# Kernel tuning notes

Hardware: AMD Instinct MI355X
Metric: run time of the kernel (lower is better)

Reference implementation:

```python
import jax, jax.numpy as jnp
import numpy as np

NUM_HEADS = 4
NUM_GROUPS = 8
EPS = 1e-5


def setup_inputs() -> dict:
    key = jax.random.key(0)
    ks = jax.random.split(key, 7)
    B, C, T, H, W = 2, 256, 16, 16, 16
    return {
        "x": jax.random.normal(ks[0], (B, C, T, H, W), dtype=jnp.float32),
        "norm_w": jax.random.normal(ks[1], (C,), dtype=jnp.float32),
        "norm_b": jax.random.normal(ks[2], (C,), dtype=jnp.float32),
        "qkv_w": jax.random.normal(ks[3], (3 * C, C), dtype=jnp.float32) * (C ** -0.5),
        "qkv_b": jax.random.normal(ks[4], (3 * C,), dtype=jnp.float32) * 0.02,
        "proj_w": jax.random.normal(ks[5], (C, C), dtype=jnp.float32) * (C ** -0.5),
        "proj_b": jax.random.normal(ks[6], (C,), dtype=jnp.float32) * 0.02,
    }


def reference(x, norm_w, norm_b, qkv_w, qkv_b, proj_w, proj_b):
    B, C, T, H, W = x.shape
    N = T * H * W
    hd = C // NUM_HEADS  # head dim

    # GroupNorm(8, C): stats over (C//G, T, H, W) per group
    xg = x.reshape(B, NUM_GROUPS, -1)
    mean = jnp.mean(xg, axis=-1, keepdims=True)
    var = jnp.var(xg, axis=-1, keepdims=True)
    xn = ((xg - mean) * jax.lax.rsqrt(var + EPS)).reshape(B, C, N)
    xn = xn * norm_w[None, :, None] + norm_b[None, :, None]

    # 1x1 conv3d qkv == per-token linear: (B, 3C, N)
    qkv = jnp.einsum('oc,bcn->bon', qkv_w, xn) + qkv_b[None, :, None]
    # reshape(B,3,heads,hd,N).permute(1,0,2,4,3) -> (3, B, heads, N, hd)
    qkv = qkv.reshape(B, 3, NUM_HEADS, hd, N).transpose(1, 0, 2, 4, 3)
    q, k, v = qkv[0], qkv[1], qkv[2]

    scale = hd ** -0.5
    scores = jnp.einsum('bhnd,bhmd->bhnm', q, k) * scale  # (B, heads, N, N)
    attn = jax.nn.softmax(scores, axis=-1)
    h = jnp.einsum('bhnm,bhmd->bhnd', attn, v)  # (B, heads, N, hd)

    # permute(0,1,3,2).reshape(B, C, T, H, W) -> channels-first tokens
    h = h.transpose(0, 1, 3, 2).reshape(B, C, N)
    out = jnp.einsum('oc,bcn->bon', proj_w, h) + proj_b[None, :, None]
    return out.reshape(B, C, T, H, W) + x
```

## Files before the change

### kernel.cpp

```cpp
#include <hip/hip_runtime.h>
#include <math.h>

#define B_DIM 2
#define C_DIM 256
#define N_TOK 4096
#define HEADS 4
#define HD 64
#define GROUPS 8
#define CPG (C_DIM / GROUPS)
#define EPS 1e-5f
#define PSB 72
#define QK_SCALE 0.180336880f
#define KSPLIT 4
#define NKT (N_TOK / 64)
#define QBLK 256
#define NQKVW (3 * C_DIM * C_DIM)
#define NPROJW (C_DIM * C_DIM)

typedef __bf16 bf16x8 __attribute__((ext_vector_type(8)));
typedef float  f32x4  __attribute__((ext_vector_type(4)));
typedef unsigned short u16x4v __attribute__((ext_vector_type(4)));
typedef unsigned short u16x8v __attribute__((ext_vector_type(8)));

__device__ __forceinline__ unsigned short f2bf(float f) {
    return __builtin_bit_cast(unsigned short, (__bf16)f);
}
__device__ __forceinline__ float bf2f(unsigned short u) {
    return (float)__builtin_bit_cast(__bf16, u);
}
__device__ __forceinline__ float exp2_fast(float x) { return __builtin_amdgcn_exp2f(x); }

__device__ __forceinline__ void gload16(const unsigned short* g, unsigned short* l) {
    __builtin_amdgcn_global_load_lds(
        (const __attribute__((address_space(1))) unsigned int*)g,
        (__attribute__((address_space(3))) unsigned int*)l, 16, 0, 0);
}

__device__ __forceinline__ int kperm(int r) {
    return (r & 0x23) | ((r & 0x0C) << 1) | ((r & 0x10) >> 2);
}

__global__ __launch_bounds__(256) void gn_part_kernel(const float* __restrict__ x,
                                                      const float* __restrict__ qkv_w,
                                                      const float* __restrict__ proj_w,
                                                      float* __restrict__ partials,
                                                      unsigned short* __restrict__ wbf) {
    const int bg = blockIdx.x >> 6, ch = blockIdx.x & 63;
    const float4* p = (const float4*)(x + (size_t)bg * CPG * N_TOK) + ch * 512;
    float s = 0.f, ss = 0.f;
#pragma unroll
    for (int r = 0; r < 2; ++r) {
        float4 v = p[threadIdx.x + (r << 8)];
        s  += v.x + v.y + v.z + v.w;
        ss += v.x * v.x + v.y * v.y + v.z * v.z + v.w * v.w;
    }
#pragma unroll
    for (int off = 32; off > 0; off >>= 1) {
        s  += __shfl_down(s, off);
        ss += __shfl_down(ss, off);
    }
    __shared__ float ls[4], lss[4];
    const int lane = threadIdx.x & 63, wid = threadIdx.x >> 6;
    if (lane == 0) { ls[wid] = s; lss[wid] = ss; }

    const int widx = blockIdx.x * 256 + threadIdx.x;
    float wv = (widx < NQKVW) ? qkv_w[widx] : proj_w[widx - NQKVW];
    wbf[widx] = f2bf(wv);

    __syncthreads();
    if (threadIdx.x == 0) {
        partials[blockIdx.x * 2 + 0] = ls[0] + ls[1] + ls[2] + ls[3];
        partials[blockIdx.x * 2 + 1] = lss[0] + lss[1] + lss[2] + lss[3];
    }
}

__global__ __launch_bounds__(256) void qkv_gemm_kernel(
    const float* __restrict__ x, const float* __restrict__ partials,
    const float* __restrict__ norm_w, const float* __restrict__ norm_b,
    const unsigned short* __restrict__ wqbf, const float* __restrict__ qkv_b,
    unsigned short* __restrict__ qkvb) {
    __shared__ unsigned short Ws[64][64];
    __shared__ unsigned short Xt[64][PSB];
    __shared__ float stat_s[GROUPS][2];
    const int n0 = blockIdx.x * 64;
    const int o0 = blockIdx.y * 64;
    const int b  = blockIdx.z;
    const int tid = threadIdx.x;
    const int lane = tid & 63, w = tid >> 6;
    const int lo = lane & 15, hi = lane >> 4;
    const int srow8 = lane >> 3, sblk = lane & 7;
    const int c16s = (sblk ^ srow8) * 8;
    int rcol[2];
#pragma unroll
    for (int c = 0; c < 2; ++c) rcol[c] = (((c * 4 + hi) ^ (lo & 7)) << 3);

    {
        const int g = tid >> 5, sub = tid & 31;
        const float* pp = partials + (((size_t)b * GROUPS + g) * 64 + sub * 2) * 2;
        float4 v = *(const float4*)pp;
        float s = v.x + v.z, ss = v.y + v.w;
#pragma unroll
        for (int off = 16; off > 0; off >>= 1) {
            s  += __shfl_down(s, off, 32);
            ss += __shfl_down(ss, off, 32);
        }
        if (sub == 0) {
            const float inv = 1.f / (float)(CPG * N_TOK);
            float mean = s * inv;
            float var  = ss * inv - mean * mean;
            stat_s[g][0] = mean;
            stat_s[g][1] = rsqrtf(var + EPS);
        }
        __syncthreads();
    }

    f32x4 acc[4] = {};
    for (int k0 = 0; k0 < C_DIM; k0 += 64) {
#pragma unroll
        for (int i = 0; i < 2; ++i) {
            int row = i * 32 + w * 8 + srow8;
            gload16(wqbf + (size_t)(o0 + row) * C_DIM + k0 + c16s, &Ws[i * 32 + w * 8][0]);
        }
#pragma unroll
        for (int r = 0; r < 4; ++r) {
            int idx = tid + (r << 8);
            int crow = idx >> 4, col4 = (idx & 15) << 2;
            int c = k0 + crow;
            int g = c >> 5;
            float ww = norm_w[c] * stat_s[g][1];
            float bb = norm_b[c] - stat_s[g][0] * ww;
            float4 v = *(const float4*)(x + ((size_t)b * C_DIM + c) * N_TOK + n0 + col4);
            Xt[col4 + 0][crow] = f2bf(v.x * ww + bb);
            Xt[col4 + 1][crow] = f2bf(v.y * ww + bb);
            Xt[col4 + 2][crow] = f2bf(v.z * ww + bb);
            Xt[col4 + 3][crow] = f2bf(v.w * ww + bb);
        }
        __syncthreads();
#pragma unroll
        for (int ck = 0; ck < 2; ++ck) {
            bf16x8 aw = *(const bf16x8*)&Ws[w * 16 + lo][rcol[ck]];
#pragma unroll
            for (int nb = 0; nb < 4; ++nb)
                acc[nb] = __builtin_amdgcn_mfma_f32_16x16x32_bf16(
                    aw, *(const bf16x8*)&Xt[nb * 16 + lo][ck * 32 + hi * 8], acc[nb], 0, 0, 0);
        }
        __syncthreads();
    }

    const int sidx = o0 >> 8;
    const int head = (o0 >> 6) & 3;
    const int od = w * 16 + hi * 4;
    float bias[4];
#pragma unroll
    for (int i = 0; i < 4; ++i) bias[i] = qkv_b[o0 + od + i];
    const size_t plane = (size_t)N_TOK * HD;

    if (sidx < 2) {
        const float sc = (sidx == 0) ? QK_SCALE : 1.0f;
        unsigned short* base = qkvb + ((size_t)(sidx * B_DIM + b) * HEADS + head) * plane;
#pragma unroll
        for (int nb = 0; nb < 4; ++nb) {
            int n = n0 + nb * 16 + lo;
            u16x4v o;
#pragma unroll
            for (int i = 0; i < 4; ++i) o[i] = f2bf((acc[nb][i] + bias[i]) * sc);
            *(u16x4v*)(base + (size_t)n * HD + od) = o;
        }
    } else {
        unsigned short* base = qkvb + (size_t)2 * B_DIM * HEADS * plane
                             + ((size_t)b * HEADS + head) * plane;
#pragma unroll
        for (int nb = 0; nb < 4; ++nb)
#pragma unroll
            for (int i = 0; i < 4; ++i)
                base[(size_t)(od + i) * N_TOK + n0 + nb * 16 + lo] = f2bf(acc[nb][i] + bias[i]);
    }
}

__global__ __launch_bounds__(512, 4) void attn_kernel(const unsigned short* __restrict__ qkvb,
                                                      unsigned short* __restrict__ obuf,
                                                      float* __restrict__ rbuf) {
    const int bh = blockIdx.x & 7;
    const int ks = (blockIdx.x >> 3) & 3;
    const int q0 = (blockIdx.x >> 5) * QBLK;
    const size_t plane = (size_t)N_TOK * HD;
    const unsigned short* Qg  = qkvb + (size_t)bh * plane;
    const unsigned short* Kg  = qkvb + (size_t)(B_DIM * HEADS + bh) * plane;
    const unsigned short* Vtg = qkvb + (size_t)2 * B_DIM * HEADS * plane + (size_t)bh * plane;

    __shared__ unsigned short Ks[2][64][64];
    __shared__ unsigned short Vt[2][64][64];

    const int tid  = threadIdx.x;
    const int lane = tid & 63;
    const int wid  = tid >> 6;
    const int lo   = lane & 15;
    const int hi   = lane >> 4;

    bf16x8 qf[2][2];
#pragma unroll
    for (int f = 0; f < 2; ++f)
#pragma unroll
        for (int c = 0; c < 2; ++c)
            qf[f][c] = *(const bf16x8*)(Qg + (size_t)(q0 + wid * 32 + f * 16 + lo) * HD
                                            + c * 32 + hi * 8);

    const int srow = tid >> 3, sblk = tid & 7;
    const int c16s = (sblk ^ (srow & 7)) * 8;
    const int krow = kperm(srow);
    int rcol[2];
#pragma unroll
    for (int c = 0; c < 2; ++c) rcol[c] = (((c * 4 + hi) ^ (lo & 7)) << 3);

#define STAGE_KV(bufi, kbase)                                                          \
    do {                                                                               \
        gload16(Kg + (size_t)((kbase) + krow) * HD + c16s, &Ks[bufi][wid * 8][0]);     \
        gload16(Vtg + (size_t)srow * N_TOK + (kbase) + c16s, &Vt[bufi][wid * 8][0]);   \
    } while (0)

    const int kt0 = ks * (NKT / KSPLIT), ktE = kt0 + NKT / KSPLIT;

    f32x4 acc[2][4] = {};
    float m[2] = {-1e30f, -1e30f}, l[2] = {0.f, 0.f};

    STAGE_KV(0, kt0 * 64);
    __syncthreads();

    for (int kt = kt0; kt < ktE; ++kt) {
        const int cur = kt & 1;
        if (kt + 1 < ktE) STAGE_KV(cur ^ 1, (kt + 1) * 64);

        f32x4 s4[2][4] = {};
        __builtin_amdgcn_s_setprio(1);
#pragma unroll
        for (int kb = 0; kb < 4; ++kb)
#pragma unroll
            for (int c = 0; c < 2; ++c) {
                bf16x8 kf = *(const bf16x8*)&Ks[cur][kb * 16 + lo][rcol[c]];
                s4[0][kb] = __builtin_amdgcn_mfma_f32_16x16x32_bf16(kf, qf[0][c], s4[0][kb], 0, 0, 0);
                s4[1][kb] = __builtin_amdgcn_mfma_f32_16x16x32_bf16(kf, qf[1][c], s4[1][kb], 0, 0, 0);
            }
        __builtin_amdgcn_s_setprio(0);

        bf16x8 pf[2][2];
#pragma unroll
        for (int f = 0; f < 2; ++f) {
            float r0 = fmaxf(fmaxf(fmaxf(s4[f][0][0], s4[f][0][1]), s4[f][0][2]), s4[f][0][3]);
            float r1 = fmaxf(fmaxf(fmaxf(s4[f][1][0], s4[f][1][1]), s4[f][1][2]), s4[f][1][3]);
            float r2 = fmaxf(fmaxf(fmaxf(s4[f][2][0], s4[f][2][1]), s4[f][2][2]), s4[f][2][3]);
            float r3 = fmaxf(fmaxf(fmaxf(s4[f][3][0], s4[f][3][1]), s4[f][3][2]), s4[f][3][3]);
            float rm = fmaxf(fmaxf(fmaxf(r0, r1), r2), r3);

            if (__any(rm > m[f] + 8.0f)) {
                float rmx = rm;
                rmx = fmaxf(rmx, __shfl_xor(rmx, 16));
                rmx = fmaxf(rmx, __shfl_xor(rmx, 32));
                const float mn = fmaxf(m[f], rmx);
                const float fi = exp2_fast(m[f] - mn);
                m[f] = mn;
                l[f] *= fi;
#pragma unroll
                for (int db = 0; db < 4; ++db)
#pragma unroll
                    for (int i = 0; i < 4; ++i) acc[f][db][i] *= fi;
            }

            float p[4][4];
            float ps = 0.f;
#pragma unroll
            for (int kb = 0; kb < 4; ++kb)
#pragma unroll
                for (int i = 0; i < 4; ++i) {
                    p[kb][i] = exp2_fast(s4[f][kb][i] - m[f]);
                    ps += p[kb][i];
                }
            l[f] += ps;

#pragma unroll
            for (int c = 0; c < 2; ++c)
#pragma unroll
                for (int j = 0; j < 8; ++j) pf[f][c][j] = (__bf16)p[2 * c + (j >> 2)][j & 3];
        }

        __builtin_amdgcn_s_setprio(1);
#pragma unroll
        for (int db = 0; db < 4; ++db)
#pragma unroll
            for (int c = 0; c < 2; ++c) {
                bf16x8 vf = *(const bf16x8*)&Vt[cur][db * 16 + lo][rcol[c]];
                acc[0][db] = __builtin_amdgcn_mfma_f32_16x16x32_bf16(vf, pf[0][c], acc[0][db], 0, 0, 0);
                acc[1][db] = __builtin_amdgcn_mfma_f32_16x16x32_bf16(vf, pf[1][c], acc[1][db], 0, 0, 0);
            }
        __builtin_amdgcn_s_setprio(0);

        __syncthreads();
    }
#undef STAGE_KV

#pragma unroll
    for (int f = 0; f < 2; ++f) {
        float l1 = l[f] + __shfl_xor(l[f], 16);
        float lt = l1 + __shfl_xor(l1, 32);
        const float inv = 1.f / lt;
        const int n = q0 + wid * 32 + f * 16 + lo;
        unsigned short* ob = obuf + ((size_t)(ks * 8 + bh) * N_TOK + n) * HD;
#pragma unroll
        for (int db = 0; db < 4; ++db) {
            u16x4v o;
#pragma unroll
            for (int i = 0; i < 4; ++i) o[i] = f2bf(acc[f][db][i] * inv);
            *(u16x4v*)(ob + db * 16 + hi * 4) = o;
        }
        if (hi == 0)
            rbuf[(size_t)(ks * 8 + bh) * N_TOK + n] = m[f] + __builtin_amdgcn_logf(lt);
    }
}

__global__ __launch_bounds__(256) void proj_kernel(
    const unsigned short* __restrict__ obuf, const float* __restrict__ rbuf,
    const unsigned short* __restrict__ wpbf, const float* __restrict__ proj_b,
    const float* __restrict__ x, float* __restrict__ out) {
    __shared__ unsigned short Ws[64][64];
    __shared__ unsigned short Hs[64][PSB];
    const int n0 = blockIdx.x * 64;
    const int o0 = blockIdx.y * 64;
    const int b  = blockIdx.z;
    const int tid = threadIdx.x;
    const int lane = tid & 63, w = tid >> 6;
    const int lo = lane & 15, hi = lane >> 4;
    const int srow8 = lane >> 3, sblk = lane & 7;
    const int c16s = (sblk ^ srow8) * 8;
    int rcol[2];
#pragma unroll
    for (int c = 0; c < 2; ++c) rcol[c] = (((c * 4 + hi) ^ (lo & 7)) << 3);

    f32x4 acc[4] = {};
    for (int k0 = 0; k0 < C_DIM; k0 += 64) {
#pragma unroll
        for (int i = 0; i < 2; ++i) {
            int row = i * 32 + w * 8 + srow8;
            gload16(wpbf + (size_t)(o0 + row) * C_DIM + k0 + c16s, &Ws[i * 32 + w * 8][0]);
        }
        {
            const int head = k0 >> 6;
            const int bh = b * HEADS + head;
#pragma unroll
            for (int r = 0; r < 2; ++r) {
                int idx = tid + (r << 8);
                int row = idx >> 3, blk = idx & 7;
                int n = n0 + row;
                float rr[KSPLIT], M = -1e30f;
#pragma unroll
                for (int k = 0; k < KSPLIT; ++k) {
                    rr[k] = rbuf[(size_t)(k * 8 + bh) * N_TOK + n];
                    M = fmaxf(M, rr[k]);
                }
                float wk[KSPLIT], tot = 0.f;
#pragma unroll
                for (int k = 0; k < KSPLIT; ++k) { wk[k] = exp2_fast(rr[k] - M); tot += wk[k]; }
                const float inv = 1.f / tot;
                float a[8] = {};
#pragma unroll
                for (int k = 0; k < KSPLIT; ++k) {
                    u16x8v v = *(const u16x8v*)(obuf
                        + ((size_t)(k * 8 + bh) * N_TOK + n) * HD + blk * 8);
#pragma unroll
                    for (int j = 0; j < 8; ++j) a[j] += wk[k] * bf2f(v[j]);
                }
                u16x8v o;
#pragma unroll
                for (int j = 0; j < 8; ++j) o[j] = f2bf(a[j] * inv);
                *(u16x8v*)&Hs[row][blk * 8] = o;
            }
        }
        __syncthreads();
#pragma unroll
        for (int ck = 0; ck < 2; ++ck) {
            bf16x8 aw = *(const bf16x8*)&Ws[w * 16 + lo][rcol[ck]];
#pragma unroll
            for (int nb = 0; nb < 4; ++nb)
                acc[nb] = __builtin_amdgcn_mfma_f32_16x16x32_bf16(
                    aw, *(const bf16x8*)&Hs[nb * 16 + lo][ck * 32 + hi * 8], acc[nb], 0, 0, 0);
        }
        __syncthreads();
    }

#pragma unroll
    for (int nb = 0; nb < 4; ++nb) {
#pragma unroll
        for (int i = 0; i < 4; ++i) {
            int o = o0 + w * 16 + hi * 4 + i;
            size_t addr = ((size_t)b * C_DIM + o) * N_TOK + n0 + nb * 16 + lo;
            out[addr] = acc[nb][i] + proj_b[o] + x[addr];
        }
    }
}

extern "C" void kernel_launch(void* const* d_in, const int* in_sizes, int n_in,
                              void* d_out, int out_size, void* d_ws, size_t ws_size,
                              hipStream_t stream) {
    const float* x      = (const float*)d_in[0];
    const float* norm_w = (const float*)d_in[1];
    const float* norm_b = (const float*)d_in[2];
    const float* qkv_w  = (const float*)d_in[3];
    const float* qkv_b  = (const float*)d_in[4];
    const float* proj_w = (const float*)d_in[5];
    const float* proj_b = (const float*)d_in[6];
    float* out = (float*)d_out;

    float* partials = (float*)d_ws;
    unsigned short* wbf = (unsigned short*)(partials + 2048);
    unsigned short* qkvb = wbf + (NQKVW + NPROJW);
    unsigned short* obuf = qkvb + (size_t)3 * B_DIM * HEADS * N_TOK * HD;
    float* rbuf = (float*)(obuf + (size_t)KSPLIT * B_DIM * HEADS * N_TOK * HD);
    const unsigned short* wqbf = wbf;
    const unsigned short* wpbf = wbf + NQKVW;

    gn_part_kernel<<<B_DIM * GROUPS * 64, 256, 0, stream>>>(x, qkv_w, proj_w, partials, wbf);
    qkv_gemm_kernel<<<dim3(N_TOK / 64, 3 * C_DIM / 64, B_DIM), 256, 0, stream>>>(
        x, partials, norm_w, norm_b, wqbf, qkv_b, qkvb);
    attn_kernel<<<(N_TOK / QBLK) * B_DIM * HEADS * KSPLIT, 512, 0, stream>>>(qkvb, obuf, rbuf);
    proj_kernel<<<dim3(N_TOK / 64, C_DIM / 64, B_DIM), 256, 0, stream>>>(
        obuf, rbuf, wpbf, proj_b, x, out);
}
```

Measured before the change: 87.84 us.

## Split GroupNorm apply into separate kernel writing token-major bf16 activations

Moves the normalize-and-transpose of x out of the QKV GEMM into a new kernel that writes a token-major bf16 buffer once. The GEMM then loads both operands with async 16-byte loads into swizzled shared memory, instead of redoing the fp32 normalization for every output tile (12 times per input). This adds a kernel launch and an extra write and read of the bf16 buffer in workspace.

```diff
diff --git a/kernel.cpp b/kernel.cpp
--- a/kernel.cpp
+++ b/kernel.cpp
@@ -74,14 +74,68 @@
     }
 }
 
-__global__ __launch_bounds__(256) void qkv_gemm_kernel(
-    const float* __restrict__ x, const float* __restrict__ partials,
-    const float* __restrict__ norm_w, const float* __restrict__ norm_b,
-    const unsigned short* __restrict__ wqbf, const float* __restrict__ qkv_b,
-    unsigned short* __restrict__ qkvb) {
-    __shared__ unsigned short Ws[64][64];
+__global__ __launch_bounds__(256) void xnorm_kernel(const float* __restrict__ x,
+                                                    const float* __restrict__ partials,
+                                                    const float* __restrict__ norm_w,
+                                                    const float* __restrict__ norm_b,
+                                                    unsigned short* __restrict__ xnT) {
     __shared__ unsigned short Xt[64][PSB];
     __shared__ float stat_s[GROUPS][2];
+    const int n0 = blockIdx.x * 64;
+    const int c0 = blockIdx.y * 64;
+    const int b  = blockIdx.z;
+    const int tid = threadIdx.x;
+
+    {
+        const int g = tid >> 5, sub = tid & 31;
+        const float* pp = partials + (((size_t)b * GROUPS + g) * 64 + sub * 2) * 2;
+        float4 v = *(const float4*)pp;
+        float s = v.x + v.z, ss = v.y + v.w;
+#pragma unroll
+        for (int off = 16; off > 0; off >>= 1) {
+            s  += __shfl_down(s, off, 32);
+            ss += __shfl_down(ss, off, 32);
+        }
+        if (sub == 0) {
+            const float inv = 1.f / (float)(CPG * N_TOK);
+            float mean = s * inv;
+            float var  = ss * inv - mean * mean;
+            stat_s[g][0] = mean;
+            stat_s[g][1] = rsqrtf(var + EPS);
+        }
+        __syncthreads();
+    }
+
+#pragma unroll
+    for (int r = 0; r < 4; ++r) {
+        int idx = tid + (r << 8);
+        int crow = idx >> 4, col4 = (idx & 15) << 2;
+        int c = c0 + crow;
+        int g = c >> 5;
+        float ww = norm_w[c] * stat_s[g][1];
+        float bb = norm_b[c] - stat_s[g][0] * ww;
+        float4 v = *(const float4*)(x + ((size_t)b * C_DIM + c) * N_TOK + n0 + col4);
+        Xt[col4 + 0][crow] = f2bf(v.x * ww + bb);
+        Xt[col4 + 1][crow] = f2bf(v.y * ww + bb);
+        Xt[col4 + 2][crow] = f2bf(v.z * ww + bb);
+        Xt[col4 + 3][crow] = f2bf(v.w * ww + bb);
+    }
+    __syncthreads();
+
+#pragma unroll
+    for (int r = 0; r < 2; ++r) {
+        int idx = tid + (r << 8);
+        int row = idx >> 3, blk = idx & 7;
+        *(u16x8v*)(xnT + ((size_t)b * N_TOK + n0 + row) * C_DIM + c0 + blk * 8) =
+            *(const u16x8v*)&Xt[row][blk * 8];
+    }
+}
+
+__global__ __launch_bounds__(256) void qkv_gemm_kernel(
+    const unsigned short* __restrict__ xnT, const unsigned short* __restrict__ wqbf,
+    const float* __restrict__ qkv_b, unsigned short* __restrict__ qkvb) {
+    __shared__ unsigned short Ws[64][64];
+    __shared__ unsigned short Xs[64][64];
     const int n0 = blockIdx.x * 64;
     const int o0 = blockIdx.y * 64;
     const int b  = blockIdx.z;
@@ -94,46 +148,14 @@
 #pragma unroll
     for (int c = 0; c < 2; ++c) rcol[c] = (((c * 4 + hi) ^ (lo & 7)) << 3);
 
-    {
-        const int g = tid >> 5, sub = tid & 31;
-        const float* pp = partials + (((size_t)b * GROUPS + g) * 64 + sub * 2) * 2;
-        float4 v = *(const float4*)pp;
-        float s = v.x + v.z, ss = v.y + v.w;
-#pragma unroll
-        for (int off = 16; off > 0; off >>= 1) {
-            s  += __shfl_down(s, off, 32);
-            ss += __shfl_down(ss, off, 32);
-        }
-        if (sub == 0) {
-            const float inv = 1.f / (float)(CPG * N_TOK);
-            float mean = s * inv;
-            float var  = ss * inv - mean * mean;
-            stat_s[g][0] = mean;
-            stat_s[g][1] = rsqrtf(var + EPS);
-        }
-        __syncthreads();
-    }
-
     f32x4 acc[4] = {};
     for (int k0 = 0; k0 < C_DIM; k0 += 64) {
 #pragma unroll
         for (int i = 0; i < 2; ++i) {
             int row = i * 32 + w * 8 + srow8;
             gload16(wqbf + (size_t)(o0 + row) * C_DIM + k0 + c16s, &Ws[i * 32 + w * 8][0]);
-        }
-#pragma unroll
-        for (int r = 0; r < 4; ++r) {
-            int idx = tid + (r << 8);
-            int crow = idx >> 4, col4 = (idx & 15) << 2;
-            int c = k0 + crow;
-            int g = c >> 5;
-            float ww = norm_w[c] * stat_s[g][1];
-            float bb = norm_b[c] - stat_s[g][0] * ww;
-            float4 v = *(const float4*)(x + ((size_t)b * C_DIM + c) * N_TOK + n0 + col4);
-            Xt[col4 + 0][crow] = f2bf(v.x * ww + bb);
-            Xt[col4 + 1][crow] = f2bf(v.y * ww + bb);
-            Xt[col4 + 2][crow] = f2bf(v.z * ww + bb);
-            Xt[col4 + 3][crow] = f2bf(v.w * ww + bb);
+            gload16(xnT + ((size_t)b * N_TOK + n0 + row) * C_DIM + k0 + c16s,
+                    &Xs[i * 32 + w * 8][0]);
         }
         __syncthreads();
 #pragma unroll
@@ -142,7 +164,7 @@
 #pragma unroll
             for (int nb = 0; nb < 4; ++nb)
                 acc[nb] = __builtin_amdgcn_mfma_f32_16x16x32_bf16(
-                    aw, *(const bf16x8*)&Xt[nb * 16 + lo][ck * 32 + hi * 8], acc[nb], 0, 0, 0);
+                    aw, *(const bf16x8*)&Xs[nb * 16 + lo][rcol[ck]], acc[nb], 0, 0, 0);
         }
         __syncthreads();
     }
@@ -410,15 +432,18 @@
 
     float* partials = (float*)d_ws;
     unsigned short* wbf = (unsigned short*)(partials + 2048);
-    unsigned short* qkvb = wbf + (NQKVW + NPROJW);
+    unsigned short* xnT = wbf + (NQKVW + NPROJW);
+    unsigned short* qkvb = xnT + (size_t)B_DIM * N_TOK * C_DIM;
     unsigned short* obuf = qkvb + (size_t)3 * B_DIM * HEADS * N_TOK * HD;
     float* rbuf = (float*)(obuf + (size_t)KSPLIT * B_DIM * HEADS * N_TOK * HD);
     const unsigned short* wqbf = wbf;
     const unsigned short* wpbf = wbf + NQKVW;
 
     gn_part_kernel<<<B_DIM * GROUPS * 64, 256, 0, stream>>>(x, qkv_w, proj_w, partials, wbf);
+    xnorm_kernel<<<dim3(N_TOK / 64, C_DIM / 64, B_DIM), 256, 0, stream>>>(
+        x, partials, norm_w, norm_b, xnT);
     qkv_gemm_kernel<<<dim3(N_TOK / 64, 3 * C_DIM / 64, B_DIM), 256, 0, stream>>>(
-        x, partials, norm_w, norm_b, wqbf, qkv_b, qkvb);
+        xnT, wqbf, qkv_b, qkvb);
     attn_kernel<<<(N_TOK / QBLK) * B_DIM * HEADS * KSPLIT, 512, 0, stream>>>(qkvb, obuf, rbuf);
     proj_kernel<<<dim3(N_TOK / 64, C_DIM / 64, B_DIM), 256, 0, stream>>>(
         obuf, rbuf, wpbf, proj_b, x, out);
```

Measured after the change: 80.63 us. -8.2%, faster.
